# Optimization experiments

Hardware: AMD Instinct MI355X
Metric: run time of the kernel (lower is better)

Reference implementation:

```python
import jax, jax.numpy as jnp
import numpy as np

D_MODEL = 1024
NUM_HEAD = 16
HEAD_DIM = D_MODEL // NUM_HEAD  # 64


def setup_inputs() -> dict:
    key = jax.random.key(0)
    ks = jax.random.split(key, 9)
    B, S = 2, 2048
    s = 0.02
    return {
        "x": jax.random.normal(ks[0], (B, S, D_MODEL), dtype=jnp.float32),
        "Wq": jax.random.normal(ks[1], (D_MODEL, D_MODEL), dtype=jnp.float32) * s,
        "bq": jax.random.normal(ks[2], (D_MODEL,), dtype=jnp.float32) * s,
        "Wk": jax.random.normal(ks[3], (D_MODEL, D_MODEL), dtype=jnp.float32) * s,
        "bk": jax.random.normal(ks[4], (D_MODEL,), dtype=jnp.float32) * s,
        "Wv": jax.random.normal(ks[5], (D_MODEL, D_MODEL), dtype=jnp.float32) * s,
        "bv": jax.random.normal(ks[6], (D_MODEL,), dtype=jnp.float32) * s,
        "Wo": jax.random.normal(ks[7], (D_MODEL, D_MODEL), dtype=jnp.float32) * s,
        "bo": jax.random.normal(ks[8], (D_MODEL,), dtype=jnp.float32) * s,
    }


def _split_head(t):
    # [B,S,D] -> [B,H,S,hd]
    B, S, _ = t.shape
    return t.reshape(B, S, NUM_HEAD, HEAD_DIM).transpose(0, 2, 1, 3)


def reference(x, Wq, bq, Wk, bk, Wv, bv, Wo, bo):
    B, S, D = x.shape
    q = _split_head(x @ Wq.T + bq)  # [B,H,S,hd]
    k = _split_head(x @ Wk.T + bk)
    v = _split_head(x @ Wv.T + bv)
    scale = 1.0 / jnp.sqrt(jnp.asarray(HEAD_DIM, dtype=x.dtype))
    scores = jnp.einsum("bhqd,bhkd->bhqk", q, k) * scale  # [B,H,S,S]
    attn = jax.nn.softmax(scores, axis=-1)
    out = jnp.einsum("bhqk,bhkd->bhqd", attn, v)  # [B,H,S,hd]
    out = out.transpose(0, 2, 1, 3).reshape(B, S, D)
    return out @ Wo.T + bo
```

## Files before the change

### kernel.cpp

```cpp
#include <hip/hip_runtime.h>
#include <cstdint>


typedef unsigned short ush;
typedef __bf16 bf16x8 __attribute__((ext_vector_type(8)));
typedef float f32x4 __attribute__((ext_vector_type(4)));
typedef ush u16x8 __attribute__((ext_vector_type(8)));
typedef ush u16x4 __attribute__((ext_vector_type(4)));
typedef unsigned int u32x4 __attribute__((ext_vector_type(4)));

__device__ __forceinline__ ush f2bf(float f) {
  unsigned int u = __float_as_uint(f);
  u += 0x7fffu + ((u >> 16) & 1u);
  return (ush)(u >> 16);
}

__device__ __forceinline__ unsigned int cvtpk2bf(float a, float b) {
  unsigned int r;
  asm("v_cvt_pk_bf16_f32 %0, %1, %2" : "=v"(r) : "v"(a), "v"(b));
  return r;
}

__device__ __forceinline__ bf16x8 bc8(u16x8 v) {
  return __builtin_bit_cast(bf16x8, v);
}

__device__ __forceinline__ void async16(const void* g, void* l) {
  __builtin_amdgcn_global_load_lds(
      (const __attribute__((address_space(1))) unsigned int*)(uintptr_t)g,
      (__attribute__((address_space(3))) unsigned int*)(uintptr_t)l, 16, 0, 0);
}

__global__ __launch_bounds__(256) void convert_kernel(
    const float* __restrict__ x, const float* __restrict__ Wq,
    const float* __restrict__ Wk, const float* __restrict__ Wv,
    const float* __restrict__ Wo,
    ush* __restrict__ xb, ush* __restrict__ Wqb, ush* __restrict__ Wkb,
    ush* __restrict__ Wvb, ush* __restrict__ Wob)
{
  int tid = blockIdx.x * 256 + threadIdx.x;
  int base = tid * 4;
  const float* src; ush* dst; int idx;
  if (base < 4194304) { src = x; dst = xb; idx = base; }
  else {
    int r = base - 4194304;
    int seg = r >> 20;
    idx = r & 1048575;
    src = seg == 0 ? Wq : seg == 1 ? Wk : seg == 2 ? Wv : Wo;
    dst = seg == 0 ? Wqb : seg == 1 ? Wkb : seg == 2 ? Wvb : Wob;
  }
  float4 f = *(const float4*)(src + idx);
  u16x4 u = { f2bf(f.x), f2bf(f.y), f2bf(f.z), f2bf(f.w) };
  *(u16x4*)(dst + idx) = u;
}

__device__ __forceinline__ void gemm128_core(
    const ush* __restrict__ gA, const ush* __restrict__ gB,
    int m0, int n0, ush* lA, ush* lB, f32x4 (&acc)[4][4])
{
  const int t = threadIdx.x, w = t >> 6, lane = t & 63;
  const int l15 = lane & 15, quad = lane >> 4;
  const int wm = (w >> 1) * 64, wn = (w & 1) * 64;
#pragma unroll
  for (int i = 0; i < 4; ++i)
#pragma unroll
    for (int j = 0; j < 4; ++j) acc[i][j] = (f32x4){0.f, 0.f, 0.f, 0.f};

  for (int kt = 0; kt < 1024; kt += 64) {
#pragma unroll
    for (int i = 0; i < 4; ++i) {
      int j = i * 256 + w * 64 + lane;
      int row = j >> 3, cc = (j & 7) ^ (row & 7);
      async16(gA + (size_t)(m0 + row) * 1024 + kt + cc * 8,
              lA + (i * 256 + w * 64) * 8);
    }
#pragma unroll
    for (int i = 0; i < 4; ++i) {
      int j = i * 256 + w * 64 + lane;
      int row = j >> 3, cc = (j & 7) ^ (row & 7);
      async16(gB + (size_t)(n0 + row) * 1024 + kt + cc * 8,
              lB + (i * 256 + w * 64) * 8);
    }
    __syncthreads();
#pragma unroll
    for (int kf = 0; kf < 2; ++kf) {
      bf16x8 aF[4], bF[4];
#pragma unroll
      for (int mt = 0; mt < 4; ++mt) {
        int row = wm + mt * 16 + l15;
        aF[mt] = bc8(*(const u16x8*)(lA + row * 64 + (((kf * 4 + quad) ^ (row & 7)) * 8)));
      }
#pragma unroll
      for (int nt = 0; nt < 4; ++nt) {
        int row = wn + nt * 16 + l15;
        bF[nt] = bc8(*(const u16x8*)(lB + row * 64 + (((kf * 4 + quad) ^ (row & 7)) * 8)));
      }
#pragma unroll
      for (int mt = 0; mt < 4; ++mt)
#pragma unroll
        for (int nt = 0; nt < 4; ++nt)
          acc[mt][nt] = __builtin_amdgcn_mfma_f32_16x16x32_bf16(
              aF[mt], bF[nt], acc[mt][nt], 0, 0, 0);
    }
    __syncthreads();
  }
}

__global__ __launch_bounds__(256, 2) void qkv_gemm(
    const ush* __restrict__ xb, const ush* __restrict__ Wqb,
    const ush* __restrict__ Wkb, const ush* __restrict__ Wvb,
    const float* __restrict__ bq, const float* __restrict__ bk,
    const float* __restrict__ bv,
    ush* __restrict__ q, ush* __restrict__ k, ush* __restrict__ vt)
{
  int bid = blockIdx.x;
  int wsel = bid >> 8;
  int rem = bid & 255;
  int m0 = (rem & 31) * 128;
  int n0 = (rem >> 5) * 128;
  const ush* gB = wsel == 0 ? Wqb : wsel == 1 ? Wkb : Wvb;
  const float* bias = wsel == 0 ? bq : wsel == 1 ? bk : bv;
  const float oscale = wsel == 1 ? 0.180336880f : 1.0f;

  __shared__ alignas(16) ush lA[128 * 64];
  __shared__ alignas(16) ush lB[128 * 64];
  f32x4 acc[4][4];
  gemm128_core(xb, gB, m0, n0, lA, lB, acc);

  const int t = threadIdx.x, w = t >> 6, lane = t & 63;
  const int l15 = lane & 15, quad = lane >> 4;
  const int wm = (w >> 1) * 64, wn = (w & 1) * 64;
  if (wsel == 2) {
#pragma unroll
    for (int nt = 0; nt < 4; ++nt) {
      int o = n0 + wn + nt * 16 + l15;
      float bl = bias[o];
      int h = o >> 6, d = o & 63;
#pragma unroll
      for (int mt = 0; mt < 4; ++mt) {
        int tb = m0 + wm + mt * 16 + quad * 4;
        int b = tb >> 11, s = tb & 2047;
        int so = s & 63;
        int sp = (s & ~63) | (so & 35) | ((so & 12) << 1) | ((so & 16) >> 2);
        u16x4 pk = { f2bf(acc[mt][nt][0] + bl), f2bf(acc[mt][nt][1] + bl),
                     f2bf(acc[mt][nt][2] + bl), f2bf(acc[mt][nt][3] + bl) };
        *(u16x4*)(vt + (size_t)(((b * 16 + h) * 64) + d) * 2048 + sp) = pk;
      }
    }
  } else {
    ush* dst = wsel == 0 ? q : k;
#pragma unroll
    for (int nt = 0; nt < 4; ++nt) {
      int o = n0 + wn + nt * 16 + l15;
      float bl = bias[o];
      int h = o >> 6, d = o & 63;
#pragma unroll
      for (int mt = 0; mt < 4; ++mt)
#pragma unroll
        for (int r = 0; r < 4; ++r) {
          int token = m0 + wm + mt * 16 + quad * 4 + r;
          int b = token >> 11, s = token & 2047;
          dst[(size_t)(((b * 16 + h) * 2048) + s) * 64 + d] =
              f2bf((acc[mt][nt][r] + bl) * oscale);
        }
    }
  }
}

__global__ __launch_bounds__(512, 4) void attn_kernel(
    const ush* __restrict__ Q, const ush* __restrict__ K,
    const ush* __restrict__ VT, ush* __restrict__ O)
{
  const int bid = blockIdx.x;
  const int bh = bid & 31;
  const int qt = bid >> 5;
  const ush* qb = Q + (size_t)bh * 2048 * 64;
  const ush* kb = K + (size_t)bh * 2048 * 64;
  const ush* vtb = VT + (size_t)bh * 64 * 2048;
  const int t = threadIdx.x, w = t >> 6, lane = t & 63;
  const int wk = w & 1, wq = w >> 1;
  const int l15 = lane & 15, quad = lane >> 4;
  const int q0 = qt * 128 + wq * 32;

  __shared__ alignas(16) ush smem[17408];
  ush* lKb = smem;
  ush* lVb = smem + 8192;

  const int r0 = t >> 3;
  const int c0 = (t & 7) ^ (r0 & 7);
  const ush* kSrc = kb + (size_t)r0 * 64 + c0 * 8;
  const ush* vSrc = vtb + (size_t)r0 * 2048 + c0 * 8;

  bf16x8 qF[2][2];
#pragma unroll
  for (int g = 0; g < 2; ++g)
#pragma unroll
    for (int kf = 0; kf < 2; ++kf)
      qF[g][kf] = bc8(*(const u16x8*)(qb + (size_t)(q0 + g * 16 + l15) * 64 +
                                      kf * 32 + quad * 8));

  const u16x8 onesU = { 0x3F80, 0x3F80, 0x3F80, 0x3F80,
                        0x3F80, 0x3F80, 0x3F80, 0x3F80 };
  const bf16x8 aOnes = bc8(onesU);

  f32x4 accO[2][4];
  f32x4 accLi[2];
#pragma unroll
  for (int g = 0; g < 2; ++g) {
    accLi[g] = (f32x4){0.f, 0.f, 0.f, 0.f};
#pragma unroll
    for (int dt = 0; dt < 4; ++dt) accO[g][dt] = (f32x4){0.f, 0.f, 0.f, 0.f};
  }

  async16(kSrc, lKb + t * 8);
  async16(vSrc, lVb + t * 8);
  __syncthreads();

  for (int it = 0; it < 32; ++it) {
    const int cur = it & 1, nxt = cur ^ 1;
    if (it + 1 < 32) {
      async16(kSrc + (size_t)(it + 1) * 4096, lKb + nxt * 4096 + t * 8);
      async16(vSrc + (it + 1) * 64,           lVb + nxt * 4096 + t * 8);
    }
    const ush* lk = lKb + cur * 4096;
    const ush* lv = lVb + cur * 4096;

    f32x4 sc[2][2];
#pragma unroll
    for (int g = 0; g < 2; ++g)
#pragma unroll
      for (int mt = 0; mt < 2; ++mt) sc[g][mt] = (f32x4){0.f, 0.f, 0.f, 0.f};
    __builtin_amdgcn_s_setprio(1);
#pragma unroll
    for (int kf = 0; kf < 2; ++kf) {
#pragma unroll
      for (int mt = 0; mt < 2; ++mt) {
        int row = (2 * wk + mt) * 16 + l15;
        bf16x8 aK = bc8(*(const u16x8*)(lk + row * 64 + (((kf * 4 + quad) ^ (row & 7)) * 8)));
#pragma unroll
        for (int g = 0; g < 2; ++g)
          sc[g][mt] = __builtin_amdgcn_mfma_f32_16x16x32_bf16(
              aK, qF[g][kf], sc[g][mt], 0, 0, 0);
      }
    }
    __builtin_amdgcn_s_setprio(0);

#pragma unroll
    for (int g = 0; g < 2; ++g)
#pragma unroll
      for (int mt = 0; mt < 2; ++mt)
#pragma unroll
        for (int r = 0; r < 4; ++r)
          sc[g][mt][r] = __builtin_amdgcn_exp2f(sc[g][mt][r]);

    bf16x8 aV[4];
#pragma unroll
    for (int dt = 0; dt < 4; ++dt)
      aV[dt] = bc8(*(const u16x8*)(lv + (dt * 16 + l15) * 64 +
                                   (((wk * 4 + quad) ^ (l15 & 7)) * 8)));
    __builtin_amdgcn_s_setprio(1);
#pragma unroll
    for (int g = 0; g < 2; ++g) {
      u32x4 bw = { cvtpk2bf(sc[g][0][0], sc[g][0][1]),
                   cvtpk2bf(sc[g][0][2], sc[g][0][3]),
                   cvtpk2bf(sc[g][1][0], sc[g][1][1]),
                   cvtpk2bf(sc[g][1][2], sc[g][1][3]) };
      bf16x8 bP = __builtin_bit_cast(bf16x8, bw);
      accLi[g] = __builtin_amdgcn_mfma_f32_16x16x32_bf16(
          aOnes, bP, accLi[g], 0, 0, 0);
#pragma unroll
      for (int dt = 0; dt < 4; ++dt)
        accO[g][dt] = __builtin_amdgcn_mfma_f32_16x16x32_bf16(
            aV[dt], bP, accO[g][dt], 0, 0, 0);
    }
    __builtin_amdgcn_s_setprio(0);
    __syncthreads();
  }

  float* redO = (float*)smem;
  float* redL = (float*)(smem + 16384);
  const int b = bh >> 4, h = bh & 15;
#define SEND_GROUP(GL)                                                       \
  {                                                                          \
    const int Gs = 2 * wq + (GL);                                            \
    _Pragma("unroll")                                                        \
    for (int dt = 0; dt < 4; ++dt)                                           \
      *(f32x4*)(redO + ((Gs * 4 + dt) * 64 + lane) * 4) = accO[GL][dt];      \
    redL[Gs * 64 + lane] = accLi[GL][0];                                     \
  }
#define FINISH_GROUP(GL)                                                     \
  {                                                                          \
    const int Gf = 2 * wq + (GL);                                            \
    _Pragma("unroll")                                                        \
    for (int dt = 0; dt < 4; ++dt)                                           \
      accO[GL][dt] += *(const f32x4*)(redO + ((Gf * 4 + dt) * 64 + lane) * 4);\
    float lsum = accLi[GL][0] + redL[Gf * 64 + lane];                        \
    const float linv = __builtin_amdgcn_rcpf(lsum);                          \
    const int s = q0 + (GL) * 16 + l15;                                      \
    _Pragma("unroll")                                                        \
    for (int dt = 0; dt < 4; ++dt) {                                         \
      u16x4 pk = { f2bf(accO[GL][dt][0] * linv), f2bf(accO[GL][dt][1] * linv),\
                   f2bf(accO[GL][dt][2] * linv), f2bf(accO[GL][dt][3] * linv)};\
      *(u16x4*)(O + (size_t)(b * 2048 + s) * 1024 + h * 64 + dt * 16 +       \
                quad * 4) = pk;                                              \
    }                                                                        \
  }
  if (wk == 0) { SEND_GROUP(1); } else { SEND_GROUP(0); }
  __syncthreads();
  if (wk == 0) { FINISH_GROUP(0); } else { FINISH_GROUP(1); }
#undef SEND_GROUP
#undef FINISH_GROUP
}

__global__ __launch_bounds__(256, 2) void out_gemm(
    const ush* __restrict__ ab, const ush* __restrict__ Wob,
    const float* __restrict__ bo, float* __restrict__ out)
{
  int rem = blockIdx.x;
  int m0 = (rem & 31) * 128;
  int n0 = (rem >> 5) * 64;
  __shared__ alignas(16) ush lA[128 * 64];
  __shared__ alignas(16) ush lB[64 * 64];

  const int t = threadIdx.x, w = t >> 6, lane = t & 63;
  const int l15 = lane & 15, quad = lane >> 4;
  const int wm = (w >> 1) * 64, wn = (w & 1) * 32;

  f32x4 acc[4][2];
#pragma unroll
  for (int i = 0; i < 4; ++i)
#pragma unroll
    for (int j = 0; j < 2; ++j) acc[i][j] = (f32x4){0.f, 0.f, 0.f, 0.f};

  for (int kt = 0; kt < 1024; kt += 64) {
#pragma unroll
    for (int i = 0; i < 4; ++i) {
      int j = i * 256 + w * 64 + lane;
      int row = j >> 3, cc = (j & 7) ^ (row & 7);
      async16(ab + (size_t)(m0 + row) * 1024 + kt + cc * 8,
              lA + (i * 256 + w * 64) * 8);
    }
#pragma unroll
    for (int i = 0; i < 2; ++i) {
      int j = i * 256 + w * 64 + lane;
      int row = j >> 3, cc = (j & 7) ^ (row & 7);
      async16(Wob + (size_t)(n0 + row) * 1024 + kt + cc * 8,
              lB + (i * 256 + w * 64) * 8);
    }
    __syncthreads();
#pragma unroll
    for (int kf = 0; kf < 2; ++kf) {
      bf16x8 aF[4], bF[2];
#pragma unroll
      for (int mt = 0; mt < 4; ++mt) {
        int row = wm + mt * 16 + l15;
        aF[mt] = bc8(*(const u16x8*)(lA + row * 64 + (((kf * 4 + quad) ^ (row & 7)) * 8)));
      }
#pragma unroll
      for (int nt = 0; nt < 2; ++nt) {
        int row = wn + nt * 16 + l15;
        bF[nt] = bc8(*(const u16x8*)(lB + row * 64 + (((kf * 4 + quad) ^ (row & 7)) * 8)));
      }
#pragma unroll
      for (int mt = 0; mt < 4; ++mt)
#pragma unroll
        for (int nt = 0; nt < 2; ++nt)
          acc[mt][nt] = __builtin_amdgcn_mfma_f32_16x16x32_bf16(
              aF[mt], bF[nt], acc[mt][nt], 0, 0, 0);
    }
    __syncthreads();
  }

#pragma unroll
  for (int nt = 0; nt < 2; ++nt) {
    int o = n0 + wn + nt * 16 + l15;
    float bl = bo[o];
#pragma unroll
    for (int mt = 0; mt < 4; ++mt)
#pragma unroll
      for (int r = 0; r < 4; ++r) {
        int token = m0 + wm + mt * 16 + quad * 4 + r;
        out[(size_t)token * 1024 + o] = acc[mt][nt][r] + bl;
      }
  }
}

extern "C" void kernel_launch(void* const* d_in, const int* in_sizes, int n_in,
                              void* d_out, int out_size, void* d_ws, size_t ws_size,
                              hipStream_t stream)
{
  const float* x  = (const float*)d_in[0];
  const float* Wq = (const float*)d_in[1];
  const float* bq = (const float*)d_in[2];
  const float* Wk = (const float*)d_in[3];
  const float* bk = (const float*)d_in[4];
  const float* Wv = (const float*)d_in[5];
  const float* bv = (const float*)d_in[6];
  const float* Wo = (const float*)d_in[7];
  const float* bo = (const float*)d_in[8];
  float* out = (float*)d_out;

  char* ws = (char*)d_ws;
  ush* xb  = (ush*)(ws);
  ush* Wqb = (ush*)(ws + (size_t)( 8u << 20));
  ush* Wkb = (ush*)(ws + (size_t)(10u << 20));
  ush* Wvb = (ush*)(ws + (size_t)(12u << 20));
  ush* Wob = (ush*)(ws + (size_t)(14u << 20));
  ush* qb  = (ush*)(ws + (size_t)(16u << 20));
  ush* kb  = (ush*)(ws + (size_t)(24u << 20));
  ush* vtb = (ush*)(ws + (size_t)(32u << 20));
  ush* ab  = (ush*)(ws + (size_t)(40u << 20));

  convert_kernel<<<8192, 256, 0, stream>>>(x, Wq, Wk, Wv, Wo,
                                           xb, Wqb, Wkb, Wvb, Wob);
  qkv_gemm<<<768, 256, 0, stream>>>(xb, Wqb, Wkb, Wvb, bq, bk, bv, qb, kb, vtb);
  attn_kernel<<<512, 512, 0, stream>>>(qb, kb, vtb, ab);
  out_gemm<<<512, 256, 0, stream>>>(ab, Wob, bo, out);
}
```

Baseline: 166.2 us.

## Software-pipeline attention QK and PV across tiles with 4-stage LDS ring

```diff
diff --git a/kernel.cpp b/kernel.cpp
--- a/kernel.cpp
+++ b/kernel.cpp
@@ -38,20 +38,23 @@
     ush* __restrict__ xb, ush* __restrict__ Wqb, ush* __restrict__ Wkb,
     ush* __restrict__ Wvb, ush* __restrict__ Wob)
 {
-  int tid = blockIdx.x * 256 + threadIdx.x;
-  int base = tid * 4;
-  const float* src; ush* dst; int idx;
-  if (base < 4194304) { src = x; dst = xb; idx = base; }
-  else {
-    int r = base - 4194304;
-    int seg = r >> 20;
-    idx = r & 1048575;
-    src = seg == 0 ? Wq : seg == 1 ? Wk : seg == 2 ? Wv : Wo;
-    dst = seg == 0 ? Wqb : seg == 1 ? Wkb : seg == 2 ? Wvb : Wob;
-  }
-  float4 f = *(const float4*)(src + idx);
-  u16x4 u = { f2bf(f.x), f2bf(f.y), f2bf(f.z), f2bf(f.w) };
-  *(u16x4*)(dst + idx) = u;
+#pragma unroll
+  for (int i = 0; i < 4; ++i) {
+    int tid = blockIdx.x * 256 + threadIdx.x + i * 524288;
+    int base = tid * 4;
+    const float* src; ush* dst; int idx;
+    if (base < 4194304) { src = x; dst = xb; idx = base; }
+    else {
+      int r = base - 4194304;
+      int seg = r >> 20;
+      idx = r & 1048575;
+      src = seg == 0 ? Wq : seg == 1 ? Wk : seg == 2 ? Wv : Wo;
+      dst = seg == 0 ? Wqb : seg == 1 ? Wkb : seg == 2 ? Wvb : Wob;
+    }
+    float4 f = *(const float4*)(src + idx);
+    u16x4 u = { f2bf(f.x), f2bf(f.y), f2bf(f.z), f2bf(f.w) };
+    *(u16x4*)(dst + idx) = u;
+  }
 }
 
 __device__ __forceinline__ void gemm128_core(
@@ -182,9 +185,9 @@
   const int l15 = lane & 15, quad = lane >> 4;
   const int q0 = qt * 128 + wq * 32;
 
-  __shared__ alignas(16) ush smem[17408];
+  __shared__ alignas(16) ush smem[32768];
   ush* lKb = smem;
-  ush* lVb = smem + 8192;
+  ush* lVb = smem + 16384;
 
   const int r0 = t >> 3;
   const int c0 = (t & 7) ^ (r0 & 7);
@@ -212,70 +215,92 @@
     for (int dt = 0; dt < 4; ++dt) accO[g][dt] = (f32x4){0.f, 0.f, 0.f, 0.f};
   }
 
+#define QK_TILE(SC, lk)                                                      \
+  {                                                                          \
+    _Pragma("unroll")                                                        \
+    for (int g = 0; g < 2; ++g)                                              \
+      _Pragma("unroll")                                                      \
+      for (int mt = 0; mt < 2; ++mt) SC[g][mt] = (f32x4){0.f, 0.f, 0.f, 0.f};\
+    __builtin_amdgcn_s_setprio(1);                                           \
+    _Pragma("unroll")                                                        \
+    for (int kf = 0; kf < 2; ++kf) {                                         \
+      _Pragma("unroll")                                                      \
+      for (int mt = 0; mt < 2; ++mt) {                                       \
+        int row = (2 * wk + mt) * 16 + l15;                                  \
+        bf16x8 aK = bc8(*(const u16x8*)((lk) + row * 64 +                    \
+                        (((kf * 4 + quad) ^ (row & 7)) * 8)));               \
+        _Pragma("unroll")                                                    \
+        for (int g = 0; g < 2; ++g)                                          \
+          SC[g][mt] = __builtin_amdgcn_mfma_f32_16x16x32_bf16(               \
+              aK, qF[g][kf], SC[g][mt], 0, 0, 0);                            \
+      }                                                                      \
+    }                                                                        \
+    __builtin_amdgcn_s_setprio(0);                                           \
+  }
+
+#define EXP_PV_TILE(SC, lv)                                                  \
+  {                                                                          \
+    _Pragma("unroll")                                                        \
+    for (int g = 0; g < 2; ++g)                                              \
+      _Pragma("unroll")                                                      \
+      for (int mt = 0; mt < 2; ++mt)                                         \
+        _Pragma("unroll")                                                    \
+        for (int r = 0; r < 4; ++r)                                          \
+          SC[g][mt][r] = __builtin_amdgcn_exp2f(SC[g][mt][r]);               \
+    bf16x8 aV[4];                                                            \
+    _Pragma("unroll")                                                        \
+    for (int dt = 0; dt < 4; ++dt)                                           \
+      aV[dt] = bc8(*(const u16x8*)((lv) + (dt * 16 + l15) * 64 +             \
+                                   (((wk * 4 + quad) ^ (l15 & 7)) * 8)));    \
+    __builtin_amdgcn_s_setprio(1);                                           \
+    _Pragma("unroll")                                                        \
+    for (int g = 0; g < 2; ++g) {                                            \
+      u32x4 bw = { cvtpk2bf(SC[g][0][0], SC[g][0][1]),                       \
+                   cvtpk2bf(SC[g][0][2], SC[g][0][3]),                       \
+                   cvtpk2bf(SC[g][1][0], SC[g][1][1]),                       \
+                   cvtpk2bf(SC[g][1][2], SC[g][1][3]) };                     \
+      bf16x8 bP = __builtin_bit_cast(bf16x8, bw);                            \
+      accLi[g] = __builtin_amdgcn_mfma_f32_16x16x32_bf16(                    \
+          aOnes, bP, accLi[g], 0, 0, 0);                                     \
+      _Pragma("unroll")                                                      \
+      for (int dt = 0; dt < 4; ++dt)                                         \
+        accO[g][dt] = __builtin_amdgcn_mfma_f32_16x16x32_bf16(               \
+            aV[dt], bP, accO[g][dt], 0, 0, 0);                               \
+    }                                                                        \
+    __builtin_amdgcn_s_setprio(0);                                           \
+  }
+
   async16(kSrc, lKb + t * 8);
   async16(vSrc, lVb + t * 8);
+  async16(kSrc + 4096, lKb + 4096 + t * 8);
+  async16(vSrc + 64,   lVb + 4096 + t * 8);
   __syncthreads();
 
-  for (int it = 0; it < 32; ++it) {
-    const int cur = it & 1, nxt = cur ^ 1;
-    if (it + 1 < 32) {
-      async16(kSrc + (size_t)(it + 1) * 4096, lKb + nxt * 4096 + t * 8);
-      async16(vSrc + (it + 1) * 64,           lVb + nxt * 4096 + t * 8);
-    }
-    const ush* lk = lKb + cur * 4096;
-    const ush* lv = lVb + cur * 4096;
-
-    f32x4 sc[2][2];
-#pragma unroll
-    for (int g = 0; g < 2; ++g)
-#pragma unroll
-      for (int mt = 0; mt < 2; ++mt) sc[g][mt] = (f32x4){0.f, 0.f, 0.f, 0.f};
-    __builtin_amdgcn_s_setprio(1);
-#pragma unroll
-    for (int kf = 0; kf < 2; ++kf) {
-#pragma unroll
-      for (int mt = 0; mt < 2; ++mt) {
-        int row = (2 * wk + mt) * 16 + l15;
-        bf16x8 aK = bc8(*(const u16x8*)(lk + row * 64 + (((kf * 4 + quad) ^ (row & 7)) * 8)));
-#pragma unroll
-        for (int g = 0; g < 2; ++g)
-          sc[g][mt] = __builtin_amdgcn_mfma_f32_16x16x32_bf16(
-              aK, qF[g][kf], sc[g][mt], 0, 0, 0);
-      }
-    }
-    __builtin_amdgcn_s_setprio(0);
-
-#pragma unroll
-    for (int g = 0; g < 2; ++g)
-#pragma unroll
-      for (int mt = 0; mt < 2; ++mt)
-#pragma unroll
-        for (int r = 0; r < 4; ++r)
-          sc[g][mt][r] = __builtin_amdgcn_exp2f(sc[g][mt][r]);
-
-    bf16x8 aV[4];
-#pragma unroll
-    for (int dt = 0; dt < 4; ++dt)
-      aV[dt] = bc8(*(const u16x8*)(lv + (dt * 16 + l15) * 64 +
-                                   (((wk * 4 + quad) ^ (l15 & 7)) * 8)));
-    __builtin_amdgcn_s_setprio(1);
-#pragma unroll
-    for (int g = 0; g < 2; ++g) {
-      u32x4 bw = { cvtpk2bf(sc[g][0][0], sc[g][0][1]),
-                   cvtpk2bf(sc[g][0][2], sc[g][0][3]),
-                   cvtpk2bf(sc[g][1][0], sc[g][1][1]),
-                   cvtpk2bf(sc[g][1][2], sc[g][1][3]) };
-      bf16x8 bP = __builtin_bit_cast(bf16x8, bw);
-      accLi[g] = __builtin_amdgcn_mfma_f32_16x16x32_bf16(
-          aOnes, bP, accLi[g], 0, 0, 0);
-#pragma unroll
-      for (int dt = 0; dt < 4; ++dt)
-        accO[g][dt] = __builtin_amdgcn_mfma_f32_16x16x32_bf16(
-            aV[dt], bP, accO[g][dt], 0, 0, 0);
-    }
-    __builtin_amdgcn_s_setprio(0);
-    __syncthreads();
-  }
+  f32x4 scA[2][2], scB[2][2];
+  QK_TILE(scA, lKb);
+
+  for (int itp = 0; itp < 16; ++itp) {
+    const int e = 2 * itp;
+    const ush* lvE = lVb + ((e)     & 3) * 4096;
+    const ush* lkO = lKb + ((e + 1) & 3) * 4096;
+    const ush* lvO = lVb + ((e + 1) & 3) * 4096;
+    if (e + 2 < 32) {
+      async16(kSrc + (size_t)(e + 2) * 4096, lKb + ((e + 2) & 3) * 4096 + t * 8);
+      async16(vSrc + (e + 2) * 64,           lVb + ((e + 2) & 3) * 4096 + t * 8);
+    }
+    QK_TILE(scB, lkO);
+    EXP_PV_TILE(scA, lvE);
+    __syncthreads();
+    if (e + 3 < 32) {
+      async16(kSrc + (size_t)(e + 3) * 4096, lKb + ((e + 3) & 3) * 4096 + t * 8);
+      async16(vSrc + (e + 3) * 64,           lVb + ((e + 3) & 3) * 4096 + t * 8);
+    }
+    if (e + 2 < 32) QK_TILE(scA, lKb + ((e + 2) & 3) * 4096);
+    EXP_PV_TILE(scB, lvO);
+    __syncthreads();
+  }
+#undef QK_TILE
+#undef EXP_PV_TILE
 
   float* redO = (float*)smem;
   float* redL = (float*)(smem + 16384);
@@ -411,7 +436,7 @@
   ush* vtb = (ush*)(ws + (size_t)(32u << 20));
   ush* ab  = (ush*)(ws + (size_t)(40u << 20));
 
-  convert_kernel<<<8192, 256, 0, stream>>>(x, Wq, Wk, Wv, Wo,
+  convert_kernel<<<2048, 256, 0, stream>>>(x, Wq, Wk, Wv, Wo,
                                            xb, Wqb, Wkb, Wvb, Wob);
   qkv_gemm<<<768, 256, 0, stream>>>(xb, Wqb, Wkb, Wvb, bq, bk, bv, qb, kb, vtb);
   attn_kernel<<<512, 512, 0, stream>>>(qb, kb, vtb, ab);
```

Measured after the change: 172.6 us. 3.8% more time.
